# Performance work log

Measured on AMD Instinct MI355X. Metric: run time of the kernel, lower is better.

## Reference

```python
import jax, jax.numpy as jnp
import numpy as np

N, F_IN, HEADS, D_HEAD, HID, OUT, E = 50000, 128, 4, 64, 256, 2, 800000
NEG_SLOPE = 0.2


def setup_inputs() -> dict:
    key = jax.random.key(0)
    ks = jax.random.split(key, 12)
    x = jax.random.normal(ks[0], (N, F_IN), dtype=jnp.float32)
    edge_index = jax.random.randint(ks[1], (2, E), 0, N, dtype=jnp.int64)
    s = 0.05
    W_gat = jax.random.normal(ks[2], (F_IN, HEADS * D_HEAD), dtype=jnp.float32) * s
    att_src = jax.random.normal(ks[3], (HEADS, D_HEAD), dtype=jnp.float32) * s
    att_dst = jax.random.normal(ks[4], (HEADS, D_HEAD), dtype=jnp.float32) * s
    b_gat = jnp.zeros((HEADS * D_HEAD,), dtype=jnp.float32)
    W1 = jax.random.normal(ks[5], (HEADS * D_HEAD, HID), dtype=jnp.float32) * s
    b1 = jnp.zeros((HID,), dtype=jnp.float32)
    W2 = jax.random.normal(ks[6], (HID, HID), dtype=jnp.float32) * s
    b2 = jnp.zeros((HID,), dtype=jnp.float32)
    W3 = jax.random.normal(ks[7], (HID, OUT), dtype=jnp.float32) * s
    b3 = jnp.zeros((OUT,), dtype=jnp.float32)
    return {"x": x, "edge_index": edge_index, "W_gat": W_gat, "att_src": att_src,
            "att_dst": att_dst, "b_gat": b_gat, "W1": W1, "b1": b1,
            "W2": W2, "b2": b2, "W3": W3, "b3": b3}


def _gat(x, edge_index, W_gat, att_src, att_dst, b_gat):
    n = x.shape[0]
    loop = jnp.arange(n, dtype=edge_index.dtype)
    src = jnp.concatenate([edge_index[0], loop])  # [E+N] message sources j
    dst = jnp.concatenate([edge_index[1], loop])  # [E+N] message targets i
    h = (x @ W_gat).reshape(n, HEADS, D_HEAD)      # [N,H,D]
    a_s = jnp.einsum('nhd,hd->nh', h, att_src)     # [N,H]
    a_d = jnp.einsum('nhd,hd->nh', h, att_dst)     # [N,H]
    e = a_s[src] + a_d[dst]                        # [E',H]
    e = jax.nn.leaky_relu(e, NEG_SLOPE)
    # per-destination-node softmax over incoming edges (numerically stable)
    emax = jax.ops.segment_max(e, dst, num_segments=n)
    e = jnp.exp(e - emax[dst])
    denom = jax.ops.segment_sum(e, dst, num_segments=n)
    alpha = e / denom[dst]                         # [E',H]
    msg = h[src] * alpha[:, :, None]               # [E',H,D]
    out = jax.ops.segment_sum(msg, dst, num_segments=n)  # [N,H,D]
    return out.reshape(n, HEADS * D_HEAD) + b_gat


def reference(x, edge_index, W_gat, att_src, att_dst, b_gat, W1, b1, W2, b2, W3, b3):
    h = _gat(x, edge_index, W_gat, att_src, att_dst, b_gat)
    h = jax.nn.relu(h @ W1 + b1)
    h = jax.nn.relu(h @ W2 + b2)
    return h @ W3 + b3
```

## Files before the change

kernel.cpp:

```cpp
#include <hip/hip_runtime.h>
#include <math.h>

#define N_NODES 50000
#define NP 50048
#define F_IN 128
#define HD 256
#define HID 256
#define NE 800000
#define CAP 64
#define NEG_SLOPE 0.2f
#define G1_BLOCKS (NP / 64)
#define FILL_BLOCKS ((NE + 1023) / 1024)
#define CNT_STRIDE 16

typedef __attribute__((ext_vector_type(8))) __bf16 bf16x8;
typedef __attribute__((ext_vector_type(4))) __bf16 bf16x4;
typedef __attribute__((ext_vector_type(4))) float f32x4;

#define GLD_LDS16(g, l)                                                      \
    __builtin_amdgcn_global_load_lds(                                        \
        (const __attribute__((address_space(1))) unsigned int*)(g),          \
        (__attribute__((address_space(3))) unsigned int*)(l), 16, 0, 0)

#define PB_INIT 196
#define PB_WG   128
#define PB_W1   256
#define PB_W2   256

__global__ __launch_bounds__(256) void prep_kernel(const float* __restrict__ Wg,
                                                   const float* __restrict__ W1,
                                                   const float* __restrict__ W2,
                                                   __bf16* __restrict__ Wg_t,
                                                   __bf16* __restrict__ W1_t,
                                                   __bf16* __restrict__ W2_t,
                                                   int* __restrict__ cnt,
                                                   unsigned short* __restrict__ bucket) {
    int b = blockIdx.x, t = threadIdx.x;
    if (b < PB_INIT) {
        int n = b * 256 + t;
        if (n < N_NODES) { cnt[(size_t)n * CNT_STRIDE] = 1; bucket[n * CAP] = (unsigned short)n; }
    } else if (b < PB_INIT + PB_WG) {
        int i = (b - PB_INIT) * 256 + t;
        int m = i >> 7, k = i & 127;
        Wg_t[i] = (__bf16)Wg[(size_t)k * HD + m];
    } else if (b < PB_INIT + PB_WG + PB_W1) {
        int i = (b - PB_INIT - PB_WG) * 256 + t;
        int m = i >> 8, k = i & 255;
        W1_t[i] = (__bf16)W1[(size_t)k * HID + m];
    } else {
        int i = (b - PB_INIT - PB_WG - PB_W1) * 256 + t;
        int m = i >> 8, k = i & 255;
        W2_t[i] = (__bf16)W2[(size_t)k * HID + m];
    }
}

__global__ __launch_bounds__(256) void g1_fill_kernel(const float* __restrict__ x,
                                                      const __bf16* __restrict__ Bt,
                                                      const float* __restrict__ att_src,
                                                      const float* __restrict__ att_dst,
                                                      const int* __restrict__ ew,
                                                      __bf16* __restrict__ h,
                                                      float* __restrict__ a_s,
                                                      float* __restrict__ a_d,
                                                      int* __restrict__ cnt,
                                                      unsigned short* __restrict__ bucket) {
    __shared__ __bf16 As[64 * 32];
    __shared__ __bf16 Bs[256 * 32];

    if (blockIdx.x >= G1_BLOCKS) {
        const int base = (blockIdx.x - G1_BLOCKS) * 1024 + threadIdx.x;
        const int e0 = base, e1 = base + 256, e2 = base + 512, e3 = base + 768;
        const bool v0 = e0 < NE, v1 = e1 < NE, v2 = e2 < NE, v3 = e3 < NE;
        long long p0 = 0, p1 = 0, p2 = 0, p3 = 0;
        if (v0) p0 = *(const long long*)&ew[2 * e0];
        if (v1) p1 = *(const long long*)&ew[2 * e1];
        if (v2) p2 = *(const long long*)&ew[2 * e2];
        if (v3) p3 = *(const long long*)&ew[2 * e3];
        const int hiall = (int)(p0 >> 32) | (int)(p1 >> 32) |
                          (int)(p2 >> 32) | (int)(p3 >> 32);
        unsigned long long bal = __ballot(hiall != 0);
        int s0 = 0, s1 = 0, s2 = 0, s3 = 0, d0 = 0, d1 = 0, d2 = 0, d3 = 0;
        if (bal == 0) {
            s0 = (int)p0; s1 = (int)p1; s2 = (int)p2; s3 = (int)p3;
            if (v0) d0 = ew[2 * NE + 2 * e0];
            if (v1) d1 = ew[2 * NE + 2 * e1];
            if (v2) d2 = ew[2 * NE + 2 * e2];
            if (v3) d3 = ew[2 * NE + 2 * e3];
        } else {
            if (v0) { s0 = ew[e0]; d0 = ew[NE + e0]; }
            if (v1) { s1 = ew[e1]; d1 = ew[NE + e1]; }
            if (v2) { s2 = ew[e2]; d2 = ew[NE + e2]; }
            if (v3) { s3 = ew[e3]; d3 = ew[NE + e3]; }
        }
        int pos0 = CAP, pos1 = CAP, pos2 = CAP, pos3 = CAP;
        if (v0) pos0 = atomicAdd(&cnt[(size_t)d0 * CNT_STRIDE], 1);
        if (v1) pos1 = atomicAdd(&cnt[(size_t)d1 * CNT_STRIDE], 1);
        if (v2) pos2 = atomicAdd(&cnt[(size_t)d2 * CNT_STRIDE], 1);
        if (v3) pos3 = atomicAdd(&cnt[(size_t)d3 * CNT_STRIDE], 1);
        if (pos0 < CAP) bucket[d0 * CAP + pos0] = (unsigned short)s0;
        if (pos1 < CAP) bucket[d1 * CAP + pos1] = (unsigned short)s1;
        if (pos2 < CAP) bucket[d2 * CAP + pos2] = (unsigned short)s2;
        if (pos3 < CAP) bucket[d3 * CAP + pos3] = (unsigned short)s3;
        return;
    }

    const int t = threadIdx.x;
    const int lane = t & 63, wv = t >> 6;
    const int lr = lane & 15, q = lane >> 4, lk = q * 8;
    const int col_off = wv * 64;
    const int row0 = blockIdx.x * 64;
    const int sr = t >> 2, sk = (t & 3) * 8;
    const int arow = row0 + sr;
    const bool avalid = arow < N_NODES;

    f32x4 acc[4][4];
#pragma unroll
    for (int r = 0; r < 4; ++r)
#pragma unroll
        for (int c = 0; c < 4; ++c) acc[r][c] = f32x4{0.f, 0.f, 0.f, 0.f};

    for (int k0 = 0; k0 < F_IN; k0 += 32) {
        float4 v0 = {0, 0, 0, 0}, v1 = {0, 0, 0, 0};
        if (avalid) {
            const float* xp = &x[(size_t)arow * F_IN + k0 + sk];
            v0 = *(const float4*)xp;
            v1 = *(const float4*)(xp + 4);
        }
        bf16x8 o;
        o[0] = (__bf16)v0.x; o[1] = (__bf16)v0.y; o[2] = (__bf16)v0.z; o[3] = (__bf16)v0.w;
        o[4] = (__bf16)v1.x; o[5] = (__bf16)v1.y; o[6] = (__bf16)v1.z; o[7] = (__bf16)v1.w;
        *(bf16x8*)&As[sr * 32 + sk] = o;
#pragma unroll
        for (int s = 0; s < 4; ++s) {
            int r = s * 64 + sr;
            GLD_LDS16(&Bt[(size_t)r * F_IN + k0 + sk], &Bs[r * 32 + sk]);
        }
        __syncthreads();
        bf16x8 af[4], bfr[4];
#pragma unroll
        for (int i = 0; i < 4; ++i) {
            af[i]  = *(const bf16x8*)&As[(i * 16 + lr) * 32 + lk];
            bfr[i] = *(const bf16x8*)&Bs[(col_off + i * 16 + lr) * 32 + lk];
        }
#pragma unroll
        for (int r = 0; r < 4; ++r)
#pragma unroll
            for (int c = 0; c < 4; ++c)
                acc[r][c] = __builtin_amdgcn_mfma_f32_16x16x32_bf16(af[r], bfr[c], acc[r][c], 0, 0, 0);
        __syncthreads();
    }

    float asv[4], adv[4];
#pragma unroll
    for (int c = 0; c < 4; ++c) {
        int col = col_off + c * 16 + lr;
        asv[c] = att_src[col];
        adv[c] = att_dst[col];
    }
    float ps[4][4], pd[4][4];
#pragma unroll
    for (int r = 0; r < 4; ++r)
#pragma unroll
        for (int i = 0; i < 4; ++i) { ps[r][i] = 0.f; pd[r][i] = 0.f; }

#pragma unroll
    for (int c = 0; c < 4; ++c) {
        int col = col_off + c * 16 + lr;
#pragma unroll
        for (int r = 0; r < 4; ++r) {
#pragma unroll
            for (int i = 0; i < 4; ++i) {
                int row = row0 + r * 16 + q * 4 + i;
                float v = acc[r][c][i];
                h[(size_t)row * HD + col] = (__bf16)v;
                ps[r][i] += v * asv[c];
                pd[r][i] += v * adv[c];
            }
        }
    }
#pragma unroll
    for (int r = 0; r < 4; ++r)
#pragma unroll
        for (int i = 0; i < 4; ++i) {
#pragma unroll
            for (int m = 1; m < 16; m <<= 1) {
                ps[r][i] += __shfl_xor(ps[r][i], m);
                pd[r][i] += __shfl_xor(pd[r][i], m);
            }
        }
    if (lr == 0) {
#pragma unroll
        for (int r = 0; r < 4; ++r)
#pragma unroll
            for (int i = 0; i < 4; ++i) {
                int row = row0 + r * 16 + q * 4 + i;
                a_s[row * 4 + wv] = ps[r][i];
                a_d[row * 4 + wv] = pd[r][i];
            }
    }
}

__device__ __forceinline__ float lrelu(float v) { return v >= 0.f ? v : NEG_SLOPE * v; }

__global__ __launch_bounds__(64) void gat_aggregate_kernel(const __bf16* __restrict__ h,
                                                           const float* __restrict__ a_s,
                                                           const float* __restrict__ a_d,
                                                           const int* __restrict__ cnt,
                                                           const unsigned short* __restrict__ bucket,
                                                           const float* __restrict__ b_gat,
                                                           __bf16* __restrict__ gat) {
    __shared__ unsigned short s_src[64];
    __shared__ float s_alpha[64][4];
    const int lane = threadIdx.x;
    const int n = blockIdx.x;

    int deg = cnt[(size_t)n * CNT_STRIDE];
    if (deg > CAP) deg = CAP;
    int src = n;
    float4 e = {-1e30f, -1e30f, -1e30f, -1e30f};
    float4 ad = *(const float4*)&a_d[n * 4];
    if (lane < deg) {
        src = bucket[n * CAP + lane];
        float4 as4 = *(const float4*)&a_s[src * 4];
        e.x = lrelu(as4.x + ad.x);
        e.y = lrelu(as4.y + ad.y);
        e.z = lrelu(as4.z + ad.z);
        e.w = lrelu(as4.w + ad.w);
    }
    float4 m = e;
#pragma unroll
    for (int off = 1; off < 64; off <<= 1) {
        m.x = fmaxf(m.x, __shfl_xor(m.x, off));
        m.y = fmaxf(m.y, __shfl_xor(m.y, off));
        m.z = fmaxf(m.z, __shfl_xor(m.z, off));
        m.w = fmaxf(m.w, __shfl_xor(m.w, off));
    }
    float4 wgt = {0, 0, 0, 0};
    if (lane < deg) {
        wgt.x = __expf(e.x - m.x); wgt.y = __expf(e.y - m.y);
        wgt.z = __expf(e.z - m.z); wgt.w = __expf(e.w - m.w);
    }
    float4 s = wgt;
#pragma unroll
    for (int off = 1; off < 64; off <<= 1) {
        s.x += __shfl_xor(s.x, off); s.y += __shfl_xor(s.y, off);
        s.z += __shfl_xor(s.z, off); s.w += __shfl_xor(s.w, off);
    }
    s_src[lane] = (unsigned short)src;
    s_alpha[lane][0] = wgt.x / s.x;
    s_alpha[lane][1] = wgt.y / s.y;
    s_alpha[lane][2] = wgt.z / s.z;
    s_alpha[lane][3] = wgt.w / s.w;
    __syncthreads();

    const int half = lane >> 5;
    const int l32 = lane & 31;
    const int c0 = l32 * 8;
    const int head = l32 >> 3;
    float acc[8];
#pragma unroll
    for (int k = 0; k < 8; ++k) acc[k] = 0.f;

    const int mde = (deg + 1) & ~1;
    int j = 0;
    for (; j + 8 <= mde; j += 8) {
        int j0 = j + half, j1 = j + 2 + half, j2 = j + 4 + half, j3 = j + 6 + half;
        int s0 = s_src[j0], s1 = s_src[j1], s2 = s_src[j2], s3 = s_src[j3];
        float a0 = s_alpha[j0][head], a1 = s_alpha[j1][head];
        float a2 = s_alpha[j2][head], a3 = s_alpha[j3][head];
        bf16x8 h0 = *(const bf16x8*)&h[(size_t)s0 * HD + c0];
        bf16x8 h1 = *(const bf16x8*)&h[(size_t)s1 * HD + c0];
        bf16x8 h2 = *(const bf16x8*)&h[(size_t)s2 * HD + c0];
        bf16x8 h3 = *(const bf16x8*)&h[(size_t)s3 * HD + c0];
#pragma unroll
        for (int k = 0; k < 8; ++k)
            acc[k] += a0 * (float)h0[k] + a1 * (float)h1[k]
                    + a2 * (float)h2[k] + a3 * (float)h3[k];
    }
    for (; j < mde; j += 2) {
        int j0 = j + half;
        int s0 = s_src[j0];
        float a0 = s_alpha[j0][head];
        bf16x8 h0 = *(const bf16x8*)&h[(size_t)s0 * HD + c0];
#pragma unroll
        for (int k = 0; k < 8; ++k)
            acc[k] += a0 * (float)h0[k];
    }
#pragma unroll
    for (int k = 0; k < 8; ++k) acc[k] += __shfl_xor(acc[k], 32);

    if (half == 0) {
        float4 bg0 = *(const float4*)&b_gat[c0];
        float4 bg1 = *(const float4*)&b_gat[c0 + 4];
        bf16x8 o;
        o[0] = (__bf16)(acc[0] + bg0.x); o[1] = (__bf16)(acc[1] + bg0.y);
        o[2] = (__bf16)(acc[2] + bg0.z); o[3] = (__bf16)(acc[3] + bg0.w);
        o[4] = (__bf16)(acc[4] + bg1.x); o[5] = (__bf16)(acc[5] + bg1.y);
        o[6] = (__bf16)(acc[6] + bg1.z); o[7] = (__bf16)(acc[7] + bg1.w);
        *(bf16x8*)&gat[(size_t)n * HD + c0] = o;
    }
}

__global__ __launch_bounds__(256) void fused_mlp_kernel(const __bf16* __restrict__ A,
                                                        const __bf16* __restrict__ W1t,
                                                        const __bf16* __restrict__ W2t,
                                                        const float* __restrict__ b1,
                                                        const float* __restrict__ b2,
                                                        const float* __restrict__ W3,
                                                        const float* __restrict__ b3,
                                                        float* __restrict__ out) {
    __shared__ __bf16 As[64 * 32];
    __shared__ __bf16 Ws[256 * 32];
    __shared__ __bf16 h1s[8 * 64 * 32];
    __shared__ float s_out[64][2];
    const int t = threadIdx.x;
    const int lane = t & 63, wv = t >> 6;
    const int lr = lane & 15, q = lane >> 4, lk = q * 8;
    const int col_off = wv * 64;
    const int row0 = blockIdx.x * 64;
    const int sr = t >> 2, sk = (t & 3) * 8;

    if (t < 128) ((float*)s_out)[t] = 0.f;

    f32x4 acc[4][4];
#pragma unroll
    for (int r = 0; r < 4; ++r)
#pragma unroll
        for (int c = 0; c < 4; ++c) acc[r][c] = f32x4{0.f, 0.f, 0.f, 0.f};

    for (int k0 = 0; k0 < HD; k0 += 32) {
        GLD_LDS16(&A[(size_t)(row0 + sr) * HD + k0 + sk], &As[sr * 32 + sk]);
#pragma unroll
        for (int s = 0; s < 4; ++s) {
            int r = s * 64 + sr;
            GLD_LDS16(&W1t[(size_t)r * HD + k0 + sk], &Ws[r * 32 + sk]);
        }
        __syncthreads();
        bf16x8 af[4], bfr[4];
#pragma unroll
        for (int i = 0; i < 4; ++i) {
            af[i]  = *(const bf16x8*)&As[(i * 16 + lr) * 32 + lk];
            bfr[i] = *(const bf16x8*)&Ws[(col_off + i * 16 + lr) * 32 + lk];
        }
#pragma unroll
        for (int r = 0; r < 4; ++r)
#pragma unroll
            for (int c = 0; c < 4; ++c)
                acc[r][c] = __builtin_amdgcn_mfma_f32_16x16x32_bf16(af[r], bfr[c], acc[r][c], 0, 0, 0);
        __syncthreads();
    }
#pragma unroll
    for (int c = 0; c < 4; ++c) {
        int col = col_off + c * 16 + lr;
        float bv = b1[col];
        int cb = (col >> 5) * 2048;
        int kk = col & 31;
#pragma unroll
        for (int r = 0; r < 4; ++r)
#pragma unroll
            for (int i = 0; i < 4; ++i) {
                int row = r * 16 + q * 4 + i;
                float v = fmaxf(acc[r][c][i] + bv, 0.f);
                h1s[cb + row * 32 + kk] = (__bf16)v;
                acc[r][c][i] = 0.f;
            }
    }
    __syncthreads();

    for (int k0 = 0; k0 < HID; k0 += 32) {
#pragma unroll
        for (int s = 0; s < 4; ++s) {
            int r = s * 64 + sr;
            GLD_LDS16(&W2t[(size_t)r * HID + k0 + sk], &Ws[r * 32 + sk]);
        }
        __syncthreads();
        const int cb = (k0 >> 5) * 2048;
        bf16x8 af[4], bfr[4];
#pragma unroll
        for (int i = 0; i < 4; ++i) {
            af[i]  = *(const bf16x8*)&h1s[cb + (i * 16 + lr) * 32 + lk];
            bfr[i] = *(const bf16x8*)&Ws[(col_off + i * 16 + lr) * 32 + lk];
        }
#pragma unroll
        for (int r = 0; r < 4; ++r)
#pragma unroll
            for (int c = 0; c < 4; ++c)
                acc[r][c] = __builtin_amdgcn_mfma_f32_16x16x32_bf16(af[r], bfr[c], acc[r][c], 0, 0, 0);
        __syncthreads();
    }

    float b2v[4], w30[4], w31[4];
#pragma unroll
    for (int c = 0; c < 4; ++c) {
        int col = col_off + c * 16 + lr;
        b2v[c] = b2[col];
        w30[c] = W3[col * 2];
        w31[c] = W3[col * 2 + 1];
    }
#pragma unroll
    for (int r = 0; r < 4; ++r) {
#pragma unroll
        for (int i = 0; i < 4; ++i) {
            float o0 = 0.f, o1 = 0.f;
#pragma unroll
            for (int c = 0; c < 4; ++c) {
                float v = fmaxf(acc[r][c][i] + b2v[c], 0.f);
                o0 += v * w30[c];
                o1 += v * w31[c];
            }
#pragma unroll
            for (int m = 1; m < 16; m <<= 1) {
                o0 += __shfl_xor(o0, m);
                o1 += __shfl_xor(o1, m);
            }
            if (lr == 0) {
                int row = r * 16 + q * 4 + i;
                atomicAdd(&s_out[row][0], o0);
                atomicAdd(&s_out[row][1], o1);
            }
        }
    }
    __syncthreads();
    if (t < 128) {
        int row = t >> 1, o = t & 1;
        int g = row0 + row;
        if (g < N_NODES) out[g * 2 + o] = s_out[row][o] + b3[o];
    }
}

extern "C" void kernel_launch(void* const* d_in, const int* in_sizes, int n_in,
                              void* d_out, int out_size, void* d_ws, size_t ws_size,
                              hipStream_t stream) {
    const float* x       = (const float*)d_in[0];
    const int*   ei      = (const int*)d_in[1];
    const float* W_gat   = (const float*)d_in[2];
    const float* att_src = (const float*)d_in[3];
    const float* att_dst = (const float*)d_in[4];
    const float* b_gat   = (const float*)d_in[5];
    const float* W1      = (const float*)d_in[6];
    const float* b1      = (const float*)d_in[7];
    const float* W2      = (const float*)d_in[8];
    const float* b2      = (const float*)d_in[9];
    const float* W3      = (const float*)d_in[10];
    const float* b3      = (const float*)d_in[11];
    float* out = (float*)d_out;

    char* ws = (char*)d_ws;
    __bf16* h_bf   = (__bf16*)ws;  ws += (size_t)NP * HD * 2;
    __bf16* gat_bf = (__bf16*)ws;  ws += (size_t)NP * HD * 2;
    __bf16* Wg_t   = (__bf16*)ws;  ws += (size_t)HD * F_IN * 2;
    __bf16* W1_t   = (__bf16*)ws;  ws += (size_t)HID * HD * 2;
    __bf16* W2_t   = (__bf16*)ws;  ws += (size_t)HID * HID * 2;
    float* a_s     = (float*)ws;   ws += (size_t)NP * 4 * 4;
    float* a_d     = (float*)ws;   ws += (size_t)NP * 4 * 4;
    int* cnt       = (int*)ws;     ws += (size_t)N_NODES * CNT_STRIDE * 4;
    unsigned short* bucket = (unsigned short*)ws;
    ws += (size_t)N_NODES * CAP * 2;

    prep_kernel<<<PB_INIT + PB_WG + PB_W1 + PB_W2, 256, 0, stream>>>(
        W_gat, W1, W2, Wg_t, W1_t, W2_t, cnt, bucket);
    g1_fill_kernel<<<G1_BLOCKS + FILL_BLOCKS, 256, 0, stream>>>(
        x, Wg_t, att_src, att_dst, ei, h_bf, a_s, a_d, cnt, bucket);
    gat_aggregate_kernel<<<N_NODES, 64, 0, stream>>>(h_bf, a_s, a_d, cnt, bucket,
                                                     b_gat, gat_bf);
    fused_mlp_kernel<<<NP / 64, 256, 0, stream>>>(gat_bf, W1_t, W2_t, b1, b2, W3, b3, out);
}
```

Measured before the change: 245.8 us.

## Split GAT aggregation across column groups with two nodes per block

The aggregation kernel changes from one 64-lane block per node covering all 256 columns to blocks that each handle two nodes (one per half-wave) and one 32-column slice, eight slices per node pair. Each half-wave computes the softmax for a single head, and 8-byte loads are spread over four edge slots with shuffle reductions afterwards. The aim is more parallelism and less per-block softmax work for all four heads. In exchange, a_s, bucket and cnt are reread eight times per node, the launch has four times as many blocks, and the loads are narrower. The count stride also drops from 16 to 4, which packs counters more tightly.

```diff
diff --git a/kernel.cpp b/kernel.cpp
--- a/kernel.cpp
+++ b/kernel.cpp
@@ -11,7 +11,7 @@
 #define NEG_SLOPE 0.2f
 #define G1_BLOCKS (NP / 64)
 #define FILL_BLOCKS ((NE + 1023) / 1024)
-#define CNT_STRIDE 16
+#define CNT_STRIDE 4
 
 typedef __attribute__((ext_vector_type(8))) __bf16 bf16x8;
 typedef __attribute__((ext_vector_type(4))) __bf16 bf16x4;
@@ -209,95 +209,73 @@
                                                            const unsigned short* __restrict__ bucket,
                                                            const float* __restrict__ b_gat,
                                                            __bf16* __restrict__ gat) {
-    __shared__ unsigned short s_src[64];
-    __shared__ float s_alpha[64][4];
+    __shared__ unsigned short s_src[128];
+    __shared__ float s_alpha[128];
     const int lane = threadIdx.x;
-    const int n = blockIdx.x;
+    const int g = blockIdx.x & 7;
+    const int pair = blockIdx.x >> 3;
+    const int half = lane >> 5;
+    const int l32 = lane & 31;
+    const int n = pair * 2 + half;
+    const int head = g >> 1;
+    const int c0 = g * 32;
 
     int deg = cnt[(size_t)n * CNT_STRIDE];
     if (deg > CAP) deg = CAP;
-    int src = n;
-    float4 e = {-1e30f, -1e30f, -1e30f, -1e30f};
-    float4 ad = *(const float4*)&a_d[n * 4];
-    if (lane < deg) {
-        src = bucket[n * CAP + lane];
-        float4 as4 = *(const float4*)&a_s[src * 4];
-        e.x = lrelu(as4.x + ad.x);
-        e.y = lrelu(as4.y + ad.y);
-        e.z = lrelu(as4.z + ad.z);
-        e.w = lrelu(as4.w + ad.w);
-    }
-    float4 m = e;
-#pragma unroll
-    for (int off = 1; off < 64; off <<= 1) {
-        m.x = fmaxf(m.x, __shfl_xor(m.x, off));
-        m.y = fmaxf(m.y, __shfl_xor(m.y, off));
-        m.z = fmaxf(m.z, __shfl_xor(m.z, off));
-        m.w = fmaxf(m.w, __shfl_xor(m.w, off));
-    }
-    float4 wgt = {0, 0, 0, 0};
-    if (lane < deg) {
-        wgt.x = __expf(e.x - m.x); wgt.y = __expf(e.y - m.y);
-        wgt.z = __expf(e.z - m.z); wgt.w = __expf(e.w - m.w);
-    }
-    float4 s = wgt;
-#pragma unroll
-    for (int off = 1; off < 64; off <<= 1) {
-        s.x += __shfl_xor(s.x, off); s.y += __shfl_xor(s.y, off);
-        s.z += __shfl_xor(s.z, off); s.w += __shfl_xor(s.w, off);
-    }
-    s_src[lane] = (unsigned short)src;
-    s_alpha[lane][0] = wgt.x / s.x;
-    s_alpha[lane][1] = wgt.y / s.y;
-    s_alpha[lane][2] = wgt.z / s.z;
-    s_alpha[lane][3] = wgt.w / s.w;
+    const float ad = a_d[n * 4 + head];
+
+    int src0 = n, src1 = n;
+    float e0 = -1e30f, e1 = -1e30f;
+    if (l32 < deg) {
+        src0 = bucket[n * CAP + l32];
+        e0 = lrelu(a_s[src0 * 4 + head] + ad);
+    }
+    if (l32 + 32 < deg) {
+        src1 = bucket[n * CAP + l32 + 32];
+        e1 = lrelu(a_s[src1 * 4 + head] + ad);
+    }
+    float m = fmaxf(e0, e1);
+#pragma unroll
+    for (int off = 1; off < 32; off <<= 1) m = fmaxf(m, __shfl_xor(m, off));
+    float w0 = (l32 < deg) ? __expf(e0 - m) : 0.f;
+    float w1 = (l32 + 32 < deg) ? __expf(e1 - m) : 0.f;
+    float s = w0 + w1;
+#pragma unroll
+    for (int off = 1; off < 32; off <<= 1) s += __shfl_xor(s, off);
+    const float inv = 1.f / s;
+    s_src[half * 64 + l32] = (unsigned short)src0;
+    s_src[half * 64 + l32 + 32] = (unsigned short)src1;
+    s_alpha[half * 64 + l32] = w0 * inv;
+    s_alpha[half * 64 + l32 + 32] = w1 * inv;
     __syncthreads();
 
-    const int half = lane >> 5;
-    const int l32 = lane & 31;
-    const int c0 = l32 * 8;
-    const int head = l32 >> 3;
-    float acc[8];
-#pragma unroll
-    for (int k = 0; k < 8; ++k) acc[k] = 0.f;
-
-    const int mde = (deg + 1) & ~1;
-    int j = 0;
-    for (; j + 8 <= mde; j += 8) {
-        int j0 = j + half, j1 = j + 2 + half, j2 = j + 4 + half, j3 = j + 6 + half;
-        int s0 = s_src[j0], s1 = s_src[j1], s2 = s_src[j2], s3 = s_src[j3];
-        float a0 = s_alpha[j0][head], a1 = s_alpha[j1][head];
-        float a2 = s_alpha[j2][head], a3 = s_alpha[j3][head];
-        bf16x8 h0 = *(const bf16x8*)&h[(size_t)s0 * HD + c0];
-        bf16x8 h1 = *(const bf16x8*)&h[(size_t)s1 * HD + c0];
-        bf16x8 h2 = *(const bf16x8*)&h[(size_t)s2 * HD + c0];
-        bf16x8 h3 = *(const bf16x8*)&h[(size_t)s3 * HD + c0];
-#pragma unroll
-        for (int k = 0; k < 8; ++k)
-            acc[k] += a0 * (float)h0[k] + a1 * (float)h1[k]
-                    + a2 * (float)h2[k] + a3 * (float)h3[k];
-    }
-    for (; j < mde; j += 2) {
-        int j0 = j + half;
-        int s0 = s_src[j0];
-        float a0 = s_alpha[j0][head];
-        bf16x8 h0 = *(const bf16x8*)&h[(size_t)s0 * HD + c0];
-#pragma unroll
-        for (int k = 0; k < 8; ++k)
-            acc[k] += a0 * (float)h0[k];
-    }
-#pragma unroll
-    for (int k = 0; k < 8; ++k) acc[k] += __shfl_xor(acc[k], 32);
-
-    if (half == 0) {
-        float4 bg0 = *(const float4*)&b_gat[c0];
-        float4 bg1 = *(const float4*)&b_gat[c0 + 4];
-        bf16x8 o;
-        o[0] = (__bf16)(acc[0] + bg0.x); o[1] = (__bf16)(acc[1] + bg0.y);
-        o[2] = (__bf16)(acc[2] + bg0.z); o[3] = (__bf16)(acc[3] + bg0.w);
-        o[4] = (__bf16)(acc[4] + bg1.x); o[5] = (__bf16)(acc[5] + bg1.y);
-        o[6] = (__bf16)(acc[6] + bg1.z); o[7] = (__bf16)(acc[7] + bg1.w);
-        *(bf16x8*)&gat[(size_t)n * HD + c0] = o;
+    const int slot = l32 >> 3;
+    const int cq = l32 & 7;
+    float acc0 = 0.f, acc1 = 0.f, acc2 = 0.f, acc3 = 0.f;
+    for (int j = slot; j < deg; j += 4) {
+        int sj = s_src[half * 64 + j];
+        float aj = s_alpha[half * 64 + j];
+        bf16x4 hv = *(const bf16x4*)&h[(size_t)sj * HD + c0 + cq * 4];
+        acc0 += aj * (float)hv[0];
+        acc1 += aj * (float)hv[1];
+        acc2 += aj * (float)hv[2];
+        acc3 += aj * (float)hv[3];
+    }
+#pragma unroll
+    for (int off = 8; off <= 16; off <<= 1) {
+        acc0 += __shfl_xor(acc0, off);
+        acc1 += __shfl_xor(acc1, off);
+        acc2 += __shfl_xor(acc2, off);
+        acc3 += __shfl_xor(acc3, off);
+    }
+    if (slot == 0) {
+        const float* bg = &b_gat[c0 + cq * 4];
+        bf16x4 o;
+        o[0] = (__bf16)(acc0 + bg[0]);
+        o[1] = (__bf16)(acc1 + bg[1]);
+        o[2] = (__bf16)(acc2 + bg[2]);
+        o[3] = (__bf16)(acc3 + bg[3]);
+        *(bf16x4*)&gat[(size_t)n * HD + c0 + cq * 4] = o;
     }
 }
 
@@ -461,7 +439,7 @@
         W_gat, W1, W2, Wg_t, W1_t, W2_t, cnt, bucket);
     g1_fill_kernel<<<G1_BLOCKS + FILL_BLOCKS, 256, 0, stream>>>(
         x, Wg_t, att_src, att_dst, ei, h_bf, a_s, a_d, cnt, bucket);
-    gat_aggregate_kernel<<<N_NODES, 64, 0, stream>>>(h_bf, a_s, a_d, cnt, bucket,
-                                                     b_gat, gat_bf);
+    gat_aggregate_kernel<<<(N_NODES / 2) * 8, 64, 0, stream>>>(h_bf, a_s, a_d, cnt,
+                                                               bucket, b_gat, gat_bf);
     fused_mlp_kernel<<<NP / 64, 256, 0, stream>>>(gat_bf, W1_t, W2_t, b1, b2, W3, b3, out);
 }
```

Result: slower. 294.3 us (+19.7%).

## Fuse GAT aggregation into MLP kernel, keeping aggregated tile in LDS

Applied to the files above, without the earlier changes.

The per-node aggregation kernel is merged into the fused MLP kernel. Each 256-thread block has its four waves each aggregate 16 destination nodes and write the bf16 result into a swizzled 64x256 LDS tile, which the first GEMM then reads directly. This removes the global round trip for the aggregated features and one kernel launch. It also shrinks the count stride. The cost is fewer, heavier blocks (782 instead of 50000), which may reduce the parallelism available to hide latency on the irregular gather. LDS use per block also grows.

```diff
diff --git a/kernel.cpp b/kernel.cpp
--- a/kernel.cpp
+++ b/kernel.cpp
@@ -11,7 +11,7 @@
 #define NEG_SLOPE 0.2f
 #define G1_BLOCKS (NP / 64)
 #define FILL_BLOCKS ((NE + 1023) / 1024)
-#define CNT_STRIDE 16
+#define CNT_STRIDE 4
 
 typedef __attribute__((ext_vector_type(8))) __bf16 bf16x8;
 typedef __attribute__((ext_vector_type(4))) __bf16 bf16x4;
@@ -202,126 +202,131 @@
 
 __device__ __forceinline__ float lrelu(float v) { return v >= 0.f ? v : NEG_SLOPE * v; }
 
-__global__ __launch_bounds__(64) void gat_aggregate_kernel(const __bf16* __restrict__ h,
-                                                           const float* __restrict__ a_s,
-                                                           const float* __restrict__ a_d,
-                                                           const int* __restrict__ cnt,
-                                                           const unsigned short* __restrict__ bucket,
-                                                           const float* __restrict__ b_gat,
-                                                           __bf16* __restrict__ gat) {
-    __shared__ unsigned short s_src[64];
-    __shared__ float s_alpha[64][4];
-    const int lane = threadIdx.x;
-    const int n = blockIdx.x;
-
-    int deg = cnt[(size_t)n * CNT_STRIDE];
-    if (deg > CAP) deg = CAP;
-    int src = n;
-    float4 e = {-1e30f, -1e30f, -1e30f, -1e30f};
-    float4 ad = *(const float4*)&a_d[n * 4];
-    if (lane < deg) {
-        src = bucket[n * CAP + lane];
-        float4 as4 = *(const float4*)&a_s[src * 4];
-        e.x = lrelu(as4.x + ad.x);
-        e.y = lrelu(as4.y + ad.y);
-        e.z = lrelu(as4.z + ad.z);
-        e.w = lrelu(as4.w + ad.w);
-    }
-    float4 m = e;
-#pragma unroll
-    for (int off = 1; off < 64; off <<= 1) {
-        m.x = fmaxf(m.x, __shfl_xor(m.x, off));
-        m.y = fmaxf(m.y, __shfl_xor(m.y, off));
-        m.z = fmaxf(m.z, __shfl_xor(m.z, off));
-        m.w = fmaxf(m.w, __shfl_xor(m.w, off));
-    }
-    float4 wgt = {0, 0, 0, 0};
-    if (lane < deg) {
-        wgt.x = __expf(e.x - m.x); wgt.y = __expf(e.y - m.y);
-        wgt.z = __expf(e.z - m.z); wgt.w = __expf(e.w - m.w);
-    }
-    float4 s = wgt;
-#pragma unroll
-    for (int off = 1; off < 64; off <<= 1) {
-        s.x += __shfl_xor(s.x, off); s.y += __shfl_xor(s.y, off);
-        s.z += __shfl_xor(s.z, off); s.w += __shfl_xor(s.w, off);
-    }
-    s_src[lane] = (unsigned short)src;
-    s_alpha[lane][0] = wgt.x / s.x;
-    s_alpha[lane][1] = wgt.y / s.y;
-    s_alpha[lane][2] = wgt.z / s.z;
-    s_alpha[lane][3] = wgt.w / s.w;
-    __syncthreads();
-
-    const int half = lane >> 5;
-    const int l32 = lane & 31;
-    const int c0 = l32 * 8;
-    const int head = l32 >> 3;
-    float acc[8];
-#pragma unroll
-    for (int k = 0; k < 8; ++k) acc[k] = 0.f;
-
-    const int mde = (deg + 1) & ~1;
-    int j = 0;
-    for (; j + 8 <= mde; j += 8) {
-        int j0 = j + half, j1 = j + 2 + half, j2 = j + 4 + half, j3 = j + 6 + half;
-        int s0 = s_src[j0], s1 = s_src[j1], s2 = s_src[j2], s3 = s_src[j3];
-        float a0 = s_alpha[j0][head], a1 = s_alpha[j1][head];
-        float a2 = s_alpha[j2][head], a3 = s_alpha[j3][head];
-        bf16x8 h0 = *(const bf16x8*)&h[(size_t)s0 * HD + c0];
-        bf16x8 h1 = *(const bf16x8*)&h[(size_t)s1 * HD + c0];
-        bf16x8 h2 = *(const bf16x8*)&h[(size_t)s2 * HD + c0];
-        bf16x8 h3 = *(const bf16x8*)&h[(size_t)s3 * HD + c0];
-#pragma unroll
-        for (int k = 0; k < 8; ++k)
-            acc[k] += a0 * (float)h0[k] + a1 * (float)h1[k]
-                    + a2 * (float)h2[k] + a3 * (float)h3[k];
-    }
-    for (; j < mde; j += 2) {
-        int j0 = j + half;
-        int s0 = s_src[j0];
-        float a0 = s_alpha[j0][head];
-        bf16x8 h0 = *(const bf16x8*)&h[(size_t)s0 * HD + c0];
-#pragma unroll
-        for (int k = 0; k < 8; ++k)
-            acc[k] += a0 * (float)h0[k];
-    }
-#pragma unroll
-    for (int k = 0; k < 8; ++k) acc[k] += __shfl_xor(acc[k], 32);
-
-    if (half == 0) {
-        float4 bg0 = *(const float4*)&b_gat[c0];
-        float4 bg1 = *(const float4*)&b_gat[c0 + 4];
-        bf16x8 o;
-        o[0] = (__bf16)(acc[0] + bg0.x); o[1] = (__bf16)(acc[1] + bg0.y);
-        o[2] = (__bf16)(acc[2] + bg0.z); o[3] = (__bf16)(acc[3] + bg0.w);
-        o[4] = (__bf16)(acc[4] + bg1.x); o[5] = (__bf16)(acc[5] + bg1.y);
-        o[6] = (__bf16)(acc[6] + bg1.z); o[7] = (__bf16)(acc[7] + bg1.w);
-        *(bf16x8*)&gat[(size_t)n * HD + c0] = o;
-    }
-}
-
-__global__ __launch_bounds__(256) void fused_mlp_kernel(const __bf16* __restrict__ A,
-                                                        const __bf16* __restrict__ W1t,
-                                                        const __bf16* __restrict__ W2t,
-                                                        const float* __restrict__ b1,
-                                                        const float* __restrict__ b2,
-                                                        const float* __restrict__ W3,
-                                                        const float* __restrict__ b3,
-                                                        float* __restrict__ out) {
-    __shared__ __bf16 As[64 * 32];
+__global__ __launch_bounds__(256) void fused_gat_mlp_kernel(const __bf16* __restrict__ h,
+                                                            const float* __restrict__ a_s,
+                                                            const float* __restrict__ a_d,
+                                                            const int* __restrict__ cnt,
+                                                            const unsigned short* __restrict__ bucket,
+                                                            const float* __restrict__ b_gat,
+                                                            const __bf16* __restrict__ W1t,
+                                                            const __bf16* __restrict__ W2t,
+                                                            const float* __restrict__ b1,
+                                                            const float* __restrict__ b2,
+                                                            const float* __restrict__ W3,
+                                                            const float* __restrict__ b3,
+                                                            float* __restrict__ out) {
+    __shared__ __bf16 tile[64 * 256];
     __shared__ __bf16 Ws[256 * 32];
-    __shared__ __bf16 h1s[8 * 64 * 32];
+    __shared__ unsigned short s_src[4][64];
+    __shared__ float s_alpha[4][64][4];
     __shared__ float s_out[64][2];
+
     const int t = threadIdx.x;
     const int lane = t & 63, wv = t >> 6;
+    const int row0 = blockIdx.x * 64;
+
+    if (t < 128) ((float*)s_out)[t] = 0.f;
+
+    {
+        const int half = lane >> 5;
+        const int l32 = lane & 31;
+        const int c0 = l32 * 8;
+        const int head = l32 >> 3;
+        for (int it = 0; it < 16; ++it) {
+            const int row = wv * 16 + it;
+            const int n = row0 + row;
+            int deg = (n < N_NODES) ? cnt[(size_t)n * CNT_STRIDE] : 0;
+            if (deg > CAP) deg = CAP;
+            int src = n;
+            float4 e = {-1e30f, -1e30f, -1e30f, -1e30f};
+            float4 ad = *(const float4*)&a_d[n * 4];
+            if (lane < deg) {
+                src = bucket[n * CAP + lane];
+                float4 as4 = *(const float4*)&a_s[src * 4];
+                e.x = lrelu(as4.x + ad.x);
+                e.y = lrelu(as4.y + ad.y);
+                e.z = lrelu(as4.z + ad.z);
+                e.w = lrelu(as4.w + ad.w);
+            }
+            float4 m = e;
+#pragma unroll
+            for (int off = 1; off < 64; off <<= 1) {
+                m.x = fmaxf(m.x, __shfl_xor(m.x, off));
+                m.y = fmaxf(m.y, __shfl_xor(m.y, off));
+                m.z = fmaxf(m.z, __shfl_xor(m.z, off));
+                m.w = fmaxf(m.w, __shfl_xor(m.w, off));
+            }
+            float4 wgt = {0, 0, 0, 0};
+            if (lane < deg) {
+                wgt.x = __expf(e.x - m.x); wgt.y = __expf(e.y - m.y);
+                wgt.z = __expf(e.z - m.z); wgt.w = __expf(e.w - m.w);
+            }
+            float4 s = wgt;
+#pragma unroll
+            for (int off = 1; off < 64; off <<= 1) {
+                s.x += __shfl_xor(s.x, off); s.y += __shfl_xor(s.y, off);
+                s.z += __shfl_xor(s.z, off); s.w += __shfl_xor(s.w, off);
+            }
+            s_src[wv][lane] = (unsigned short)src;
+            s_alpha[wv][lane][0] = wgt.x / s.x;
+            s_alpha[wv][lane][1] = wgt.y / s.y;
+            s_alpha[wv][lane][2] = wgt.z / s.z;
+            s_alpha[wv][lane][3] = wgt.w / s.w;
+            asm volatile("s_waitcnt lgkmcnt(0)" ::: "memory");
+            __builtin_amdgcn_sched_barrier(0);
+
+            float acc[8];
+#pragma unroll
+            for (int k = 0; k < 8; ++k) acc[k] = 0.f;
+
+            const int mde = (deg + 1) & ~1;
+            int j = 0;
+            for (; j + 8 <= mde; j += 8) {
+                int j0 = j + half, j1 = j + 2 + half, j2 = j + 4 + half, j3 = j + 6 + half;
+                int s0 = s_src[wv][j0], s1 = s_src[wv][j1];
+                int s2 = s_src[wv][j2], s3 = s_src[wv][j3];
+                float a0 = s_alpha[wv][j0][head], a1 = s_alpha[wv][j1][head];
+                float a2 = s_alpha[wv][j2][head], a3 = s_alpha[wv][j3][head];
+                bf16x8 h0 = *(const bf16x8*)&h[(size_t)s0 * HD + c0];
+                bf16x8 h1 = *(const bf16x8*)&h[(size_t)s1 * HD + c0];
+                bf16x8 h2 = *(const bf16x8*)&h[(size_t)s2 * HD + c0];
+                bf16x8 h3 = *(const bf16x8*)&h[(size_t)s3 * HD + c0];
+#pragma unroll
+                for (int k = 0; k < 8; ++k)
+                    acc[k] += a0 * (float)h0[k] + a1 * (float)h1[k]
+                            + a2 * (float)h2[k] + a3 * (float)h3[k];
+            }
+            for (; j < mde; j += 2) {
+                int j0 = j + half;
+                int s0 = s_src[wv][j0];
+                float a0 = s_alpha[wv][j0][head];
+                bf16x8 h0 = *(const bf16x8*)&h[(size_t)s0 * HD + c0];
+#pragma unroll
+                for (int k = 0; k < 8; ++k)
+                    acc[k] += a0 * (float)h0[k];
+            }
+#pragma unroll
+            for (int k = 0; k < 8; ++k) acc[k] += __shfl_xor(acc[k], 32);
+
+            if (half == 0) {
+                float4 bg0 = *(const float4*)&b_gat[c0];
+                float4 bg1 = *(const float4*)&b_gat[c0 + 4];
+                bf16x8 o;
+                o[0] = (__bf16)(acc[0] + bg0.x); o[1] = (__bf16)(acc[1] + bg0.y);
+                o[2] = (__bf16)(acc[2] + bg0.z); o[3] = (__bf16)(acc[3] + bg0.w);
+                o[4] = (__bf16)(acc[4] + bg1.x); o[5] = (__bf16)(acc[5] + bg1.y);
+                o[6] = (__bf16)(acc[6] + bg1.z); o[7] = (__bf16)(acc[7] + bg1.w);
+                const int byte_off = row * 512 + ((l32 * 16) ^ ((row & 7) << 4));
+                *(bf16x8*)((char*)tile + byte_off) = o;
+            }
+        }
+    }
+    __syncthreads();
+
     const int lr = lane & 15, q = lane >> 4, lk = q * 8;
     const int col_off = wv * 64;
-    const int row0 = blockIdx.x * 64;
     const int sr = t >> 2, sk = (t & 3) * 8;
 
-    if (t < 128) ((float*)s_out)[t] = 0.f;
-
     f32x4 acc[4][4];
 #pragma unroll
     for (int r = 0; r < 4; ++r)
@@ -329,7 +334,6 @@
         for (int c = 0; c < 4; ++c) acc[r][c] = f32x4{0.f, 0.f, 0.f, 0.f};
 
     for (int k0 = 0; k0 < HD; k0 += 32) {
-        GLD_LDS16(&A[(size_t)(row0 + sr) * HD + k0 + sk], &As[sr * 32 + sk]);
 #pragma unroll
         for (int s = 0; s < 4; ++s) {
             int r = s * 64 + sr;
@@ -339,7 +343,9 @@
         bf16x8 af[4], bfr[4];
 #pragma unroll
         for (int i = 0; i < 4; ++i) {
-            af[i]  = *(const bf16x8*)&As[(i * 16 + lr) * 32 + lk];
+            const int ar = i * 16 + lr;
+            const int abyte = ar * 512 + ((k0 * 2 + q * 16) ^ ((ar & 7) << 4));
+            af[i]  = *(const bf16x8*)((const char*)tile + abyte);
             bfr[i] = *(const bf16x8*)&Ws[(col_off + i * 16 + lr) * 32 + lk];
         }
 #pragma unroll
@@ -361,7 +367,7 @@
             for (int i = 0; i < 4; ++i) {
                 int row = r * 16 + q * 4 + i;
                 float v = fmaxf(acc[r][c][i] + bv, 0.f);
-                h1s[cb + row * 32 + kk] = (__bf16)v;
+                tile[cb + row * 32 + kk] = (__bf16)v;
                 acc[r][c][i] = 0.f;
             }
     }
@@ -378,7 +384,7 @@
         bf16x8 af[4], bfr[4];
 #pragma unroll
         for (int i = 0; i < 4; ++i) {
-            af[i]  = *(const bf16x8*)&h1s[cb + (i * 16 + lr) * 32 + lk];
+            af[i]  = *(const bf16x8*)&tile[cb + (i * 16 + lr) * 32 + lk];
             bfr[i] = *(const bf16x8*)&Ws[(col_off + i * 16 + lr) * 32 + lk];
         }
 #pragma unroll
@@ -447,7 +453,6 @@
 
     char* ws = (char*)d_ws;
     __bf16* h_bf   = (__bf16*)ws;  ws += (size_t)NP * HD * 2;
-    __bf16* gat_bf = (__bf16*)ws;  ws += (size_t)NP * HD * 2;
     __bf16* Wg_t   = (__bf16*)ws;  ws += (size_t)HD * F_IN * 2;
     __bf16* W1_t   = (__bf16*)ws;  ws += (size_t)HID * HD * 2;
     __bf16* W2_t   = (__bf16*)ws;  ws += (size_t)HID * HID * 2;
@@ -461,7 +466,7 @@
         W_gat, W1, W2, Wg_t, W1_t, W2_t, cnt, bucket);
     g1_fill_kernel<<<G1_BLOCKS + FILL_BLOCKS, 256, 0, stream>>>(
         x, Wg_t, att_src, att_dst, ei, h_bf, a_s, a_d, cnt, bucket);
-    gat_aggregate_kernel<<<N_NODES, 64, 0, stream>>>(h_bf, a_s, a_d, cnt, bucket,
-                                                     b_gat, gat_bf);
-    fused_mlp_kernel<<<NP / 64, 256, 0, stream>>>(gat_bf, W1_t, W2_t, b1, b2, W3, b3, out);
+    fused_gat_mlp_kernel<<<NP / 64, 256, 0, stream>>>(h_bf, a_s, a_d, cnt, bucket,
+                                                      b_gat, W1_t, W2_t, b1, b2,
+                                                      W3, b3, out);
 }
```

Result: slower. 290.6 us (+18.2%).

## Prefetch first neighbor rows before softmax and write-through bucket stores

Applied to the files above, without the earlier changes.

In the aggregation kernel, the first eight neighbor feature rows are loaded right after the source indices are read, before the softmax reductions, so their memory latency overlaps the shuffle math. The first eight-edge chunk then uses these prefetched registers. Separately, bucket writes in the fill phase use inline-asm global_store_short with sc0 sc1 cache bits, likely so the stores write through the caches. The prefetch raises register pressure and adds loads for low-degree nodes (which fall back to the node itself). The inline asm ties the code to one ISA.

```diff
diff --git a/kernel.cpp b/kernel.cpp
--- a/kernel.cpp
+++ b/kernel.cpp
@@ -21,6 +21,11 @@
     __builtin_amdgcn_global_load_lds(                                        \
         (const __attribute__((address_space(1))) unsigned int*)(g),          \
         (__attribute__((address_space(3))) unsigned int*)(l), 16, 0, 0)
+
+__device__ __forceinline__ void store_u16_wt(unsigned short* p, unsigned v) {
+    unsigned long long a = (unsigned long long)p;
+    asm volatile("global_store_short %0, %1, off sc0 sc1" :: "v"(a), "v"(v) : "memory");
+}
 
 #define PB_INIT 196
 #define PB_WG   128
@@ -97,10 +102,10 @@
         if (v1) pos1 = atomicAdd(&cnt[(size_t)d1 * CNT_STRIDE], 1);
         if (v2) pos2 = atomicAdd(&cnt[(size_t)d2 * CNT_STRIDE], 1);
         if (v3) pos3 = atomicAdd(&cnt[(size_t)d3 * CNT_STRIDE], 1);
-        if (pos0 < CAP) bucket[d0 * CAP + pos0] = (unsigned short)s0;
-        if (pos1 < CAP) bucket[d1 * CAP + pos1] = (unsigned short)s1;
-        if (pos2 < CAP) bucket[d2 * CAP + pos2] = (unsigned short)s2;
-        if (pos3 < CAP) bucket[d3 * CAP + pos3] = (unsigned short)s3;
+        if (pos0 < CAP) store_u16_wt(&bucket[d0 * CAP + pos0], (unsigned)(unsigned short)s0);
+        if (pos1 < CAP) store_u16_wt(&bucket[d1 * CAP + pos1], (unsigned)(unsigned short)s1);
+        if (pos2 < CAP) store_u16_wt(&bucket[d2 * CAP + pos2], (unsigned)(unsigned short)s2);
+        if (pos3 < CAP) store_u16_wt(&bucket[d3 * CAP + pos3], (unsigned)(unsigned short)s3);
         return;
     }
 
@@ -217,11 +222,28 @@
     int deg = cnt[(size_t)n * CNT_STRIDE];
     if (deg > CAP) deg = CAP;
     int src = n;
-    float4 e = {-1e30f, -1e30f, -1e30f, -1e30f};
     float4 ad = *(const float4*)&a_d[n * 4];
+    float4 as4 = {0, 0, 0, 0};
     if (lane < deg) {
         src = bucket[n * CAP + lane];
-        float4 as4 = *(const float4*)&a_s[src * 4];
+        as4 = *(const float4*)&a_s[src * 4];
+    }
+
+    const int half = lane >> 5;
+    const int l32 = lane & 31;
+    const int c0 = l32 * 8;
+    const int head = l32 >> 3;
+    const int pj0 = __shfl(src, half);
+    const int pj1 = __shfl(src, 2 + half);
+    const int pj2 = __shfl(src, 4 + half);
+    const int pj3 = __shfl(src, 6 + half);
+    const bf16x8 hp0 = *(const bf16x8*)&h[(size_t)pj0 * HD + c0];
+    const bf16x8 hp1 = *(const bf16x8*)&h[(size_t)pj1 * HD + c0];
+    const bf16x8 hp2 = *(const bf16x8*)&h[(size_t)pj2 * HD + c0];
+    const bf16x8 hp3 = *(const bf16x8*)&h[(size_t)pj3 * HD + c0];
+
+    float4 e = {-1e30f, -1e30f, -1e30f, -1e30f};
+    if (lane < deg) {
         e.x = lrelu(as4.x + ad.x);
         e.y = lrelu(as4.y + ad.y);
         e.z = lrelu(as4.z + ad.z);
@@ -253,29 +275,36 @@
     s_alpha[lane][3] = wgt.w / s.w;
     __syncthreads();
 
-    const int half = lane >> 5;
-    const int l32 = lane & 31;
-    const int c0 = l32 * 8;
-    const int head = l32 >> 3;
     float acc[8];
 #pragma unroll
     for (int k = 0; k < 8; ++k) acc[k] = 0.f;
 
     const int mde = (deg + 1) & ~1;
     int j = 0;
-    for (; j + 8 <= mde; j += 8) {
-        int j0 = j + half, j1 = j + 2 + half, j2 = j + 4 + half, j3 = j + 6 + half;
-        int s0 = s_src[j0], s1 = s_src[j1], s2 = s_src[j2], s3 = s_src[j3];
-        float a0 = s_alpha[j0][head], a1 = s_alpha[j1][head];
-        float a2 = s_alpha[j2][head], a3 = s_alpha[j3][head];
-        bf16x8 h0 = *(const bf16x8*)&h[(size_t)s0 * HD + c0];
-        bf16x8 h1 = *(const bf16x8*)&h[(size_t)s1 * HD + c0];
-        bf16x8 h2 = *(const bf16x8*)&h[(size_t)s2 * HD + c0];
-        bf16x8 h3 = *(const bf16x8*)&h[(size_t)s3 * HD + c0];
+    if (mde >= 8) {
+        const float a0 = s_alpha[half][head];
+        const float a1 = s_alpha[2 + half][head];
+        const float a2 = s_alpha[4 + half][head];
+        const float a3 = s_alpha[6 + half][head];
 #pragma unroll
         for (int k = 0; k < 8; ++k)
-            acc[k] += a0 * (float)h0[k] + a1 * (float)h1[k]
-                    + a2 * (float)h2[k] + a3 * (float)h3[k];
+            acc[k] += a0 * (float)hp0[k] + a1 * (float)hp1[k]
+                    + a2 * (float)hp2[k] + a3 * (float)hp3[k];
+        j = 8;
+        for (; j + 8 <= mde; j += 8) {
+            int j0 = j + half, j1 = j + 2 + half, j2 = j + 4 + half, j3 = j + 6 + half;
+            int s0 = s_src[j0], s1 = s_src[j1], s2 = s_src[j2], s3 = s_src[j3];
+            float b0 = s_alpha[j0][head], b1 = s_alpha[j1][head];
+            float b2 = s_alpha[j2][head], b3 = s_alpha[j3][head];
+            bf16x8 h0 = *(const bf16x8*)&h[(size_t)s0 * HD + c0];
+            bf16x8 h1 = *(const bf16x8*)&h[(size_t)s1 * HD + c0];
+            bf16x8 h2 = *(const bf16x8*)&h[(size_t)s2 * HD + c0];
+            bf16x8 h3 = *(const bf16x8*)&h[(size_t)s3 * HD + c0];
+#pragma unroll
+            for (int k = 0; k < 8; ++k)
+                acc[k] += b0 * (float)h0[k] + b1 * (float)h1[k]
+                        + b2 * (float)h2[k] + b3 * (float)h3[k];
+        }
     }
     for (; j < mde; j += 2) {
         int j0 = j + half;
```

Result: no change. 242.7 us (-1.3%).
